# Optimization experiments

Measured on AMD Instinct MI355X. Metric: run time of the kernel, lower is better.

Reference implementation:

```python
import jax, jax.numpy as jnp
import numpy as np

B, T, C_IN, H, W = 8, 12, 64, 64, 64
HID = 128
K = 3
NUM_CLASSES = 5


def _conv2d(x, w, b):
    # x: (B, Cin, H, W), w: (Cout, Cin, k, k) -> (B, Cout, H, W), SAME padding
    y = jax.lax.conv_general_dilated(
        x, w, window_strides=(1, 1), padding='SAME',
        dimension_numbers=('NCHW', 'OIHW', 'NCHW'))
    return y + b[None, :, None, None]


def setup_inputs() -> dict:
    key = jax.random.key(0)
    ks = jax.random.split(key, 5)
    inputs = jax.random.normal(ks[0], (B, T, C_IN, H, W), dtype=jnp.float32)
    # ConvLSTM gate conv: concat(x, h) channels -> 4*hidden gate channels
    fan_in = (C_IN + HID) * K * K
    w_lstm = jax.random.normal(ks[1], (4 * HID, C_IN + HID, K, K), dtype=jnp.float32) / np.sqrt(fan_in)
    b_lstm = jnp.zeros((4 * HID,), dtype=jnp.float32)
    w_conv = jax.random.normal(ks[2], (NUM_CLASSES, HID, K, K), dtype=jnp.float32) / np.sqrt(HID * K * K)
    b_conv = jnp.zeros((NUM_CLASSES,), dtype=jnp.float32)
    return {'inputs': inputs, 'w_lstm': w_lstm, 'b_lstm': b_lstm,
            'w_conv': w_conv, 'b_conv': b_conv}


def _clstm(inputs, w_lstm, b_lstm):
    # inputs: (B, T, C, H, W); returns final hidden state (B, HID, H, W)
    xs = jnp.transpose(inputs, (1, 0, 2, 3, 4))  # (T, B, C, H, W)
    h0 = jnp.zeros((inputs.shape[0], HID, H, W), dtype=inputs.dtype)
    c0 = jnp.zeros_like(h0)

    def step(carry, x_t):
        h, c = carry
        combined = jnp.concatenate([x_t, h], axis=1)           # (B, C+HID, H, W)
        gates = _conv2d(combined, w_lstm, b_lstm)              # (B, 4*HID, H, W)
        cc_i, cc_f, cc_o, cc_g = jnp.split(gates, 4, axis=1)
        i = jax.nn.sigmoid(cc_i)
        f = jax.nn.sigmoid(cc_f)
        o = jax.nn.sigmoid(cc_o)
        g = jnp.tanh(cc_g)
        c_next = f * c + i * g
        h_next = o * jnp.tanh(c_next)
        return (h_next, c_next), None

    (h_T, _), _ = jax.lax.scan(step, (h0, c0), xs)
    return h_T


def reference(inputs, w_lstm, b_lstm, w_conv, b_conv):
    final_state = _clstm(inputs, w_lstm, b_lstm)               # (B, HID, H, W)
    scores = _conv2d(final_state, w_conv, b_conv)              # (B, NUM_CLASSES, H, W)
    # Softmax2d over channels followed by log == channelwise log_softmax
    preds = jax.nn.log_softmax(scores, axis=1)
    return preds
```

## Files before the change

kernel.cpp:

```cpp
#include <hip/hip_runtime.h>
#include <math.h>

#define BB   8
#define TT   12

typedef _Float16 f16;
typedef f16  f16x8 __attribute__((ext_vector_type(8)));
typedef float f32x4 __attribute__((ext_vector_type(4)));

#define OFF_WT2  0ull
#define OFF_WC   1818624ull
#define OFF_XP   1855488ull
#define OFF_HA   6451200ull
#define OFF_HB   15642624ull
#define OFF_C    24834048ull
#define WS_END   41611264ull
#define ZERO_BYTES (WS_END - OFF_XP)

#define A_BYTES 31680
#define B_BYTES 37888

__device__ inline void gload16(const void* g, void* l) {
    __builtin_amdgcn_global_load_lds((const __attribute__((address_space(1))) void*)g,
                                     (__attribute__((address_space(3))) void*)l, 16, 0, 0);
}

__device__ inline float sigm_fast(float x) {
    return 1.f / (1.f + __expf(-x));
}
__device__ inline float tanh_fast(float x) {
    float xx = fminf(fmaxf(x, -15.f), 15.f);
    float e = __expf(2.f * xx);
    return (e - 1.f) / (e + 1.f);
}

__global__ __launch_bounds__(256) void zero_kernel(float4* __restrict__ p, int n4) {
    int i = blockIdx.x * blockDim.x + threadIdx.x;
    int stride = gridDim.x * blockDim.x;
    for (; i < n4; i += stride) p[i] = make_float4(0.f, 0.f, 0.f, 0.f);
}

__global__ __launch_bounds__(256) void wprep(const float* __restrict__ w, f16* __restrict__ wT2) {
    int t = blockIdx.x * 256 + threadIdx.x;
    if (t >= 8 * 6 * 64 * 296) return;
    int k    = t % 296;
    int r    = t / 296;
    int co_l = r & 63;
    int r2   = r >> 6;
    int chunk = r2 % 6;
    int ntl   = r2 / 6;
    f16 val = (f16)0.f;
    if (k < 288) {
        int tap = k >> 5, ci_l = k & 31;
        int ci  = chunk * 32 + ci_l;
        int cop = ntl * 64 + co_l;
        int hid = cop >> 2, gate = cop & 3;
        val = (f16)w[((size_t)(gate * 128 + hid) * 192 + ci) * 9 + tap];
    }
    wT2[t] = val;
}

__global__ __launch_bounds__(256) void wcprep(const float* __restrict__ w, float* __restrict__ wc) {
    int t = blockIdx.x * 256 + threadIdx.x;
    if (t >= 9216) return;
    int cls = t & 7, ci = (t >> 3) & 127, tap = t >> 10;
    wc[t] = (cls < 5) ? w[(size_t)(cls * 128 + ci) * 9 + tap] : 0.f;
}

__global__ __launch_bounds__(256) void xprep(const float* __restrict__ x, f16* __restrict__ xp, int t) {
    int pos = blockIdx.x * 256 + threadIdx.x;
    int b = pos >> 12, rr = pos & 4095, y = rr >> 6, xx = rr & 63;
    const float* s = x + ((size_t)(b * TT + t) * 64) * 4096 + y * 64 + xx;
    f16* d = xp + (((size_t)b * 66 + y + 1) * 68 + xx + 1) * 64;
    #pragma unroll
    for (int c8 = 0; c8 < 8; ++c8) {
        f16x8 v;
        #pragma unroll
        for (int e = 0; e < 8; ++e) v[e] = (f16)s[(size_t)(c8 * 8 + e) * 4096];
        *(f16x8*)&d[c8 * 8] = v;
    }
}

__device__ inline float pickc(f32x4 v, int j) {
    return j == 0 ? v[0] : j == 1 ? v[1] : j == 2 ? v[2] : v[3];
}

__global__ __launch_bounds__(256, 2) void gemm_step(
    const f16* __restrict__ xp, const f16* __restrict__ hin,
    const f16* __restrict__ wT2, const float* __restrict__ b_lstm,
    float* __restrict__ c_st, f16* __restrict__ hout)
{
    __shared__ __align__(16) char smem[A_BYTES + B_BYTES];
    f16* As = (f16*)smem;
    char* Bs = smem + A_BYTES;

    const int tid  = threadIdx.x;
    const int lane = tid & 63;
    const int wid  = tid >> 6;
    const int l15  = lane & 15, lg = lane >> 4;

    const int bid = blockIdx.x;
    const int nt  = bid >> 7;
    const int mt  = bid & 127;
    const int b   = mt >> 4;
    const int yr  = (mt & 15) << 2;

    const int rowbase = (b * 66 + yr) * 68;
    const f16* wslice = wT2 + (size_t)(nt * 6) * 18944;

    f32x4 acc[4][4] = {};
    f16x8 areg[7];

    int po[7], wo[7], c8o[7];
    bool av[7];
    #pragma unroll
    for (int i = 0; i < 7; ++i) {
        int idx = i * 256 + tid;
        av[i] = idx < 1584;
        int ci8 = idx & 3;
        int pc  = idx >> 2;
        int r   = (pc * 497) >> 15;
        int c   = pc - r * 66;
        po[i]  = rowbase + r * 68 + c;
        c8o[i] = ci8 * 8;
        wo[i]  = pc * 40 + ci8 * 8;
    }

    auto loadA = [&](int cc) {
        if (cc < 2) {
            const f16* src = xp + cc * 32;
            #pragma unroll
            for (int i = 0; i < 7; ++i)
                if (av[i]) areg[i] = *(const f16x8*)(src + ((size_t)po[i] << 6) + c8o[i]);
        } else {
            const f16* src = hin + (cc * 32 - 64);
            #pragma unroll
            for (int i = 0; i < 7; ++i)
                if (av[i]) areg[i] = *(const f16x8*)(src + ((size_t)po[i] << 7) + c8o[i]);
        }
    };
    auto writeA = [&]() {
        #pragma unroll
        for (int i = 0; i < 7; ++i)
            if (av[i]) *(f16x8*)&As[wo[i]] = areg[i];
    };
    auto stageB = [&](int cc) {
        const char* bsrc = (const char*)(wslice + (size_t)cc * 18944);
        for (int k = wid; k < 37; k += 4)
            gload16(bsrc + k * 1024 + lane * 16, Bs + k * 1024);
    };
    auto compute = [&]() {
        const f16* Bsf = (const f16*)Bs;
        #pragma unroll
        for (int tap = 0; tap < 9; ++tap) {
            const int dy = tap / 3, dx = tap - dy * 3;
            f16x8 a[4];
            #pragma unroll
            for (int mf = 0; mf < 4; ++mf)
                a[mf] = *(const f16x8*)&As[((wid + dy) * 66 + mf * 16 + l15 + dx) * 40 + lg * 8];
            f16x8 bf[4];
            #pragma unroll
            for (int nf = 0; nf < 4; ++nf)
                bf[nf] = *(const f16x8*)&Bsf[(nf * 16 + l15) * 296 + tap * 32 + lg * 8];
            #pragma unroll
            for (int mf = 0; mf < 4; ++mf)
                #pragma unroll
                for (int nf = 0; nf < 4; ++nf)
                    acc[mf][nf] = __builtin_amdgcn_mfma_f32_16x16x32_f16(a[mf], bf[nf], acc[mf][nf], 0, 0, 0);
        }
    };

    loadA(0);
    stageB(0);
    writeA();
    __syncthreads();

    #pragma unroll 1
    for (int cc = 0; cc < 6; ++cc) {
        if (cc < 5) loadA(cc + 1);
        compute();
        if (cc < 5) {
            __syncthreads();
            stageB(cc + 1);
            writeA();
            __syncthreads();
        }
    }

    const int q = lane & 3;
    #pragma unroll
    for (int mf = 0; mf < 4; ++mf) {
        #pragma unroll
        for (int nf = 0; nf < 4; ++nf) {
            int hid = nt * 16 + nf * 4 + (l15 >> 2);
            float bias = b_lstm[q * 128 + hid];
            f32x4 v = acc[mf][nf];
            v[0] += bias; v[1] += bias; v[2] += bias; v[3] += bias;
            float own = pickc(v, q);
            float r1 = __shfl_xor(pickc(v, q ^ 1), 1);
            float r2 = __shfl_xor(pickc(v, q ^ 2), 2);
            float r3 = __shfl_xor(pickc(v, q ^ 3), 3);
            float gi = q == 0 ? own : (q == 1 ? r1 : q == 2 ? r2 : r3);
            float gf = q == 1 ? own : (q == 0 ? r1 : q == 3 ? r2 : r3);
            float go = q == 2 ? own : (q == 3 ? r1 : q == 0 ? r2 : r3);
            float gg = q == 3 ? own : (q == 2 ? r1 : q == 1 ? r2 : r3);
            float i_ = sigm_fast(gi);
            float f_ = sigm_fast(gf);
            float o_ = sigm_fast(go);
            float g_ = tanh_fast(gg);
            int px = mf * 16 + lg * 4 + q;
            int py = yr + wid;
            size_t ic = (((size_t)b * 64 + py) * 64 + px) * 128 + hid;
            float cv = f_ * c_st[ic] + i_ * g_;
            c_st[ic] = cv;
            float hv = o_ * tanh_fast(cv);
            hout[(((size_t)b * 66 + py + 1) * 68 + (px + 1)) * 128 + hid] = (f16)hv;
        }
    }
}

__global__ __launch_bounds__(256) void final_conv(
    const f16* __restrict__ h, const float* __restrict__ wc,
    const float* __restrict__ b_conv, float* __restrict__ out)
{
    __shared__ float swc[9216];
    for (int i = threadIdx.x; i < 9216; i += 256) swc[i] = wc[i];
    __syncthreads();
    int pos = blockIdx.x * 256 + threadIdx.x;
    int b = pos >> 12, rr = pos & 4095, y = rr >> 6, xx = rr & 63;
    float acc[5];
    #pragma unroll
    for (int cls = 0; cls < 5; ++cls) acc[cls] = b_conv[cls];
    #pragma unroll 1
    for (int tap = 0; tap < 9; ++tap) {
        int dy = tap / 3, dx = tap - dy * 3;
        const f16* hp = h + (((size_t)b * 66 + y + dy) * 68 + xx + dx) * 128;
        #pragma unroll
        for (int c16 = 0; c16 < 16; ++c16) {
            f16x8 v = *(const f16x8*)&hp[c16 * 8];
            #pragma unroll
            for (int e = 0; e < 8; ++e) {
                float hv = (float)v[e];
                const float* wp = &swc[(size_t)(tap * 128 + c16 * 8 + e) * 8];
                acc[0] = fmaf(hv, wp[0], acc[0]);
                acc[1] = fmaf(hv, wp[1], acc[1]);
                acc[2] = fmaf(hv, wp[2], acc[2]);
                acc[3] = fmaf(hv, wp[3], acc[3]);
                acc[4] = fmaf(hv, wp[4], acc[4]);
            }
        }
    }
    float m = acc[0];
    #pragma unroll
    for (int cls = 1; cls < 5; ++cls) m = fmaxf(m, acc[cls]);
    float s = 0.f;
    #pragma unroll
    for (int cls = 0; cls < 5; ++cls) s += __expf(acc[cls] - m);
    float lse = logf(s) + m;
    #pragma unroll
    for (int cls = 0; cls < 5; ++cls)
        out[((size_t)(b * 5 + cls) << 12) + (y << 6) + xx] = acc[cls] - lse;
}

extern "C" void kernel_launch(void* const* d_in, const int* in_sizes, int n_in,
                              void* d_out, int out_size, void* d_ws, size_t ws_size,
                              hipStream_t stream) {
    const float* x      = (const float*)d_in[0];
    const float* w_lstm = (const float*)d_in[1];
    const float* b_lstm = (const float*)d_in[2];
    const float* w_conv = (const float*)d_in[3];
    const float* b_conv = (const float*)d_in[4];
    char* ws = (char*)d_ws;
    f16*   wT2 = (f16*)(ws + OFF_WT2);
    float* wc  = (float*)(ws + OFF_WC);
    f16*   xp  = (f16*)(ws + OFF_XP);
    f16*   hA  = (f16*)(ws + OFF_HA);
    f16*   hB  = (f16*)(ws + OFF_HB);
    float* c   = (float*)(ws + OFF_C);

    zero_kernel<<<2048, 256, 0, stream>>>((float4*)(ws + OFF_XP), (int)(ZERO_BYTES / 16));
    wprep<<<3552, 256, 0, stream>>>(w_lstm, wT2);
    wcprep<<<36, 256, 0, stream>>>(w_conv, wc);

    for (int t = 0; t < TT; ++t) {
        const f16* hin  = (t & 1) ? hB : hA;
        f16*       hout = (t & 1) ? hA : hB;
        xprep<<<128, 256, 0, stream>>>(x, xp, t);
        gemm_step<<<1024, 256, 0, stream>>>(xp, hin, wT2, b_lstm, c, hout);
    }
    final_conv<<<128, 256, 0, stream>>>(hA, wc, b_conv, (float*)d_out);
}
```

Baseline: 947.3 us.

## Double-buffer weight slices per kernel row to overlap staging with MFMA

```diff
diff --git a/kernel.cpp b/kernel.cpp
--- a/kernel.cpp
+++ b/kernel.cpp
@@ -8,17 +8,17 @@
 typedef f16  f16x8 __attribute__((ext_vector_type(8)));
 typedef float f32x4 __attribute__((ext_vector_type(4)));
 
-#define OFF_WT2  0ull
-#define OFF_WC   1818624ull
-#define OFF_XP   1855488ull
-#define OFF_HA   6451200ull
-#define OFF_HB   15642624ull
-#define OFF_C    24834048ull
-#define WS_END   41611264ull
+#define OFF_WT3  0ull
+#define OFF_WC   1916928ull
+#define OFF_XP   1953792ull
+#define OFF_HA   6549504ull
+#define OFF_HB   15740928ull
+#define OFF_C    24932352ull
+#define WS_END   41709568ull
 #define ZERO_BYTES (WS_END - OFF_XP)
 
-#define A_BYTES 31680
-#define B_BYTES 37888
+#define A_BYTES  31680
+#define BSL_BYTES 13312
 
 __device__ inline void gload16(const void* g, void* l) {
     __builtin_amdgcn_global_load_lds((const __attribute__((address_space(1))) void*)g,
@@ -40,24 +40,25 @@
     for (; i < n4; i += stride) p[i] = make_float4(0.f, 0.f, 0.f, 0.f);
 }
 
-__global__ __launch_bounds__(256) void wprep(const float* __restrict__ w, f16* __restrict__ wT2) {
+__global__ __launch_bounds__(256) void wprep(const float* __restrict__ w, f16* __restrict__ wT3) {
     int t = blockIdx.x * 256 + threadIdx.x;
-    if (t >= 8 * 6 * 64 * 296) return;
-    int k    = t % 296;
-    int r    = t / 296;
+    if (t >= 8 * 6 * 3 * 64 * 104) return;
+    int k    = t % 104;
+    int r    = t / 104;
     int co_l = r & 63;
     int r2   = r >> 6;
-    int chunk = r2 % 6;
-    int ntl   = r2 / 6;
+    int dy    = r2 % 3;
+    int chunk = (r2 / 3) % 6;
+    int ntl   = r2 / 18;
     f16 val = (f16)0.f;
-    if (k < 288) {
-        int tap = k >> 5, ci_l = k & 31;
+    if (k < 96) {
+        int dx = k >> 5, ci_l = k & 31;
         int ci  = chunk * 32 + ci_l;
         int cop = ntl * 64 + co_l;
         int hid = cop >> 2, gate = cop & 3;
-        val = (f16)w[((size_t)(gate * 128 + hid) * 192 + ci) * 9 + tap];
-    }
-    wT2[t] = val;
+        val = (f16)w[((size_t)(gate * 128 + hid) * 192 + ci) * 9 + dy * 3 + dx];
+    }
+    wT3[t] = val;
 }
 
 __global__ __launch_bounds__(256) void wcprep(const float* __restrict__ w, float* __restrict__ wc) {
@@ -87,12 +88,13 @@
 
 __global__ __launch_bounds__(256, 2) void gemm_step(
     const f16* __restrict__ xp, const f16* __restrict__ hin,
-    const f16* __restrict__ wT2, const float* __restrict__ b_lstm,
+    const f16* __restrict__ wT3, const float* __restrict__ b_lstm,
     float* __restrict__ c_st, f16* __restrict__ hout)
 {
-    __shared__ __align__(16) char smem[A_BYTES + B_BYTES];
+    __shared__ __align__(16) char smem[A_BYTES + 2 * BSL_BYTES];
     f16* As = (f16*)smem;
-    char* Bs = smem + A_BYTES;
+    char* Bbuf0 = smem + A_BYTES;
+    char* Bbuf1 = smem + A_BYTES + BSL_BYTES;
 
     const int tid  = threadIdx.x;
     const int lane = tid & 63;
@@ -106,7 +108,7 @@
     const int yr  = (mt & 15) << 2;
 
     const int rowbase = (b * 66 + yr) * 68;
-    const f16* wslice = wT2 + (size_t)(nt * 6) * 18944;
+    const f16* wslice = wT3 + (size_t)nt * (6 * 3 * 64 * 104);
 
     f32x4 acc[4][4] = {};
     f16x8 areg[7];
@@ -144,16 +146,15 @@
         for (int i = 0; i < 7; ++i)
             if (av[i]) *(f16x8*)&As[wo[i]] = areg[i];
     };
-    auto stageB = [&](int cc) {
-        const char* bsrc = (const char*)(wslice + (size_t)cc * 18944);
-        for (int k = wid; k < 37; k += 4)
+    auto stageB = [&](int ph, char* Bs) {
+        const char* bsrc = (const char*)wslice + (size_t)ph * BSL_BYTES;
+        for (int k = wid; k < 13; k += 4)
             gload16(bsrc + k * 1024 + lane * 16, Bs + k * 1024);
     };
-    auto compute = [&]() {
+    auto compute_dy = [&](int dy, const char* Bs) {
         const f16* Bsf = (const f16*)Bs;
         #pragma unroll
-        for (int tap = 0; tap < 9; ++tap) {
-            const int dy = tap / 3, dx = tap - dy * 3;
+        for (int dx = 0; dx < 3; ++dx) {
             f16x8 a[4];
             #pragma unroll
             for (int mf = 0; mf < 4; ++mf)
@@ -161,7 +162,7 @@
             f16x8 bf[4];
             #pragma unroll
             for (int nf = 0; nf < 4; ++nf)
-                bf[nf] = *(const f16x8*)&Bsf[(nf * 16 + l15) * 296 + tap * 32 + lg * 8];
+                bf[nf] = *(const f16x8*)&Bsf[(nf * 16 + l15) * 104 + dx * 32 + lg * 8];
             #pragma unroll
             for (int mf = 0; mf < 4; ++mf)
                 #pragma unroll
@@ -171,17 +172,24 @@
     };
 
     loadA(0);
-    stageB(0);
+    stageB(0, Bbuf0);
     writeA();
     __syncthreads();
+
+    char* bufs[2] = { Bbuf0, Bbuf1 };
+    int p = 0;
 
     #pragma unroll 1
     for (int cc = 0; cc < 6; ++cc) {
         if (cc < 5) loadA(cc + 1);
-        compute();
+        #pragma unroll 1
+        for (int dy = 0; dy < 3; ++dy) {
+            if (p < 17) stageB(p + 1, bufs[(p + 1) & 1]);
+            compute_dy(dy, bufs[p & 1]);
+            __syncthreads();
+            ++p;
+        }
         if (cc < 5) {
-            __syncthreads();
-            stageB(cc + 1);
             writeA();
             __syncthreads();
         }
@@ -271,7 +279,7 @@
     const float* w_conv = (const float*)d_in[3];
     const float* b_conv = (const float*)d_in[4];
     char* ws = (char*)d_ws;
-    f16*   wT2 = (f16*)(ws + OFF_WT2);
+    f16*   wT3 = (f16*)(ws + OFF_WT3);
     float* wc  = (float*)(ws + OFF_WC);
     f16*   xp  = (f16*)(ws + OFF_XP);
     f16*   hA  = (f16*)(ws + OFF_HA);
@@ -279,14 +287,14 @@
     float* c   = (float*)(ws + OFF_C);
 
     zero_kernel<<<2048, 256, 0, stream>>>((float4*)(ws + OFF_XP), (int)(ZERO_BYTES / 16));
-    wprep<<<3552, 256, 0, stream>>>(w_lstm, wT2);
+    wprep<<<3744, 256, 0, stream>>>(w_lstm, wT3);
     wcprep<<<36, 256, 0, stream>>>(w_conv, wc);
 
     for (int t = 0; t < TT; ++t) {
         const f16* hin  = (t & 1) ? hB : hA;
         f16*       hout = (t & 1) ? hA : hB;
         xprep<<<128, 256, 0, stream>>>(x, xp, t);
-        gemm_step<<<1024, 256, 0, stream>>>(xp, hin, wT2, b_lstm, c, hout);
+        gemm_step<<<1024, 256, 0, stream>>>(xp, hin, wT3, b_lstm, c, hout);
     }
     final_conv<<<128, 256, 0, stream>>>(hA, wc, b_conv, (float*)d_out);
 }
```

After: 1.050 ms. 10.9% more time.
